# Performance work log

Hardware: AMD Instinct MI355X
Metric: run time of the kernel (lower is better)

The kernel has to match this reference:

```python
import jax, jax.numpy as jnp
import numpy as np

N_BONES = 8
NV = 14062
PARENTS = [-1, 0, 1, 2, 3, 4, 5, 6]  # kinematic chain


def rotvec_to_rotmat(rv):
    # rv: [..., 3] -> [..., 3, 3] via Rodrigues
    ang = jnp.sqrt(jnp.sum(rv * rv, axis=-1) + 1e-12)  # [...]
    k = rv / ang[..., None]
    kx, ky, kz = k[..., 0], k[..., 1], k[..., 2]
    z = jnp.zeros_like(kx)
    K = jnp.stack([
        jnp.stack([z, -kz, ky], -1),
        jnp.stack([kz, z, -kx], -1),
        jnp.stack([-ky, kx, z], -1)], -2)  # [...,3,3]
    s = jnp.sin(ang)[..., None, None]
    c = jnp.cos(ang)[..., None, None]
    I = jnp.eye(3, dtype=rv.dtype)
    return I + s * K + (1.0 - c) * (K @ K)


def bilinear_sample(img, gx, gy):
    # img: [H, W]; gx, gy: [B, Nv] normalized coords in [-1,1]
    # bilinear, border padding, align_corners=True (matches F.grid_sample)
    H, W = img.shape
    x = jnp.clip((gx + 1.0) * 0.5 * (W - 1), 0.0, W - 1.0)
    y = jnp.clip((gy + 1.0) * 0.5 * (H - 1), 0.0, H - 1.0)
    x0 = jnp.floor(x); y0 = jnp.floor(y)
    x0i = x0.astype(jnp.int32); y0i = y0.astype(jnp.int32)
    x1i = jnp.minimum(x0i + 1, W - 1); y1i = jnp.minimum(y0i + 1, H - 1)
    wx = x - x0; wy = y - y0
    v00 = img[y0i, x0i]; v01 = img[y0i, x1i]
    v10 = img[y1i, x0i]; v11 = img[y1i, x1i]
    return (v00 * (1 - wx) + v01 * wx) * (1 - wy) + (v10 * (1 - wx) + v11 * wx) * wy


def setup_inputs() -> dict:
    key = jax.random.key(0)
    ks = jax.random.split(key, 12)
    B = 256
    theta = jax.random.normal(ks[0], (B, N_BONES, 3), jnp.float32) * 0.3
    tau = jax.random.normal(ks[1], (B, 1), jnp.float32) * 0.1
    alpha = jax.random.uniform(ks[2], (B, 1), jnp.float32)
    bsw = jax.random.uniform(ks[3], (B, 55), jnp.float32)
    W = jax.random.uniform(ks[4], (N_BONES, NV), jnp.float32) + 1e-3
    W = W / W.sum(axis=0, keepdims=True)  # done in HACK.__init__
    T = jax.random.normal(ks[5], (NV, 3), jnp.float32)
    P = jax.random.normal(ks[6], (N_BONES, 3, 3, NV, 3), jnp.float32) * 0.01
    L = jax.random.uniform(ks[7], (1, 1, 256, 256), jnp.float32)
    ts = jax.random.normal(ks[8], (NV, 3), jnp.float32)
    # L2P: per-bone rigid transforms (rotation + small translation)
    rv = jax.random.normal(ks[9], (N_BONES, 3), jnp.float32) * 0.2
    R = rotvec_to_rotmat(rv)
    t = jax.random.normal(ks[10], (N_BONES, 3), jnp.float32) * 0.1
    L2P = jnp.tile(jnp.eye(4, dtype=jnp.float32), (N_BONES, 1, 1))
    L2P = L2P.at[:, :3, :3].set(R).at[:, :3, 3].set(t)
    E = jax.random.normal(ks[11], (55, NV, 3), jnp.float32) * 0.05
    uvgrid = jax.random.uniform(jax.random.fold_in(key, 99), (NV, 2), jnp.float32)
    return {"theta": theta, "tau": tau, "alpha": alpha, "bsw": bsw, "W": W,
            "T": T, "P": P, "L": L, "ts": ts, "L2P": L2P, "E": E, "uvgrid": uvgrid}


def reference(theta, tau, alpha, bsw, W, T, P, L, ts, L2P, E, uvgrid):
    B = theta.shape[0]
    R = rotvec_to_rotmat(theta)  # [B, Nb, 3, 3]
    # theta_matrix_zero: bone 0 subtracts itself (-> 0), others subtract I
    sub = jnp.concatenate([R[:, :1],
                           jnp.broadcast_to(jnp.eye(3, dtype=R.dtype), (B, N_BONES - 1, 3, 3))], axis=1)
    theta_zero = R - sub  # [B, Nb, 3, 3]
    # pose-corrective blendshapes: sum over (bone, i, j)
    P_theta = jnp.einsum('bnij,nijvk->bvk', theta_zero, P)  # [B, Nv, 3]

    # forward kinematics along chain: L2W_pose[i] = L2W_pose[parent] @ (L2P[i] @ local[i])
    local = jnp.tile(jnp.eye(4, dtype=R.dtype), (B, N_BONES, 1, 1))
    local = local.at[:, :, :3, :3].set(R)  # [B, Nb, 4, 4]
    mats = []
    for i in range(N_BONES):
        Ai = jnp.einsum('ij,bjk->bik', L2P[i], local[:, i])
        if PARENTS[i] >= 0:
            Ai = jnp.matmul(mats[PARENTS[i]], Ai)
        mats.append(Ai)
    L2W_pose = jnp.stack(mats, axis=1)  # [B, Nb, 4, 4]

    # rest-pose world-to-local (inverse bind matrices)
    rest = []
    for i in range(N_BONES):
        rest.append(L2P[i] if PARENTS[i] < 0 else rest[PARENTS[i]] @ L2P[i])
    W2L = jnp.linalg.inv(jnp.stack(rest))  # [Nb, 4, 4]

    W2L2pWs = jnp.einsum('bnij,njk->bnik', L2W_pose, W2L)  # [B, Nb, 4, 4]
    # skinning-weight contraction over bones -> per-vertex 4x4 transform
    M = jnp.einsum('bnij,nv->bvij', W2L2pWs, W)  # [B, Nv, 4, 4]

    # larynx displacement via grid_sample
    uv = uvgrid * 2.0 - 1.0  # [Nv, 2]
    gx = jnp.broadcast_to(uv[None, :, 0], (B, uv.shape[0]))
    gy = uv[None, :, 1] + tau * 2.0  # shift y by tau*2 (F.pad(tau*2,[1,0]))
    dist = bilinear_sample(L[0, 0], gx, gy)  # [B, Nv]
    L_tau = dist[:, :, None] * ts[None]  # [B, Nv, 3]

    T_theta = (T[None] + P_theta
               + jnp.einsum('bn,nvk->bvk', bsw, E)
               + L_tau * alpha[:, :, None])  # [B, Nv, 3]

    # homogeneous per-vertex 4x4 matvec, keep xyz
    T_transformed = (jnp.einsum('bvij,bvj->bvi', M[:, :, :3, :3], T_theta)
                     + M[:, :, :3, 3])
    return T_transformed
```

## Files before the change

kernel.cpp:

```cpp
#include <hip/hip_runtime.h>
#include <cmath>

#define NB     8
#define NVERT  14062
#define NV3    42186
#define BATCH  256
#define KP     63
#define KE     55
#define KPAD   120
#define KT     8
#define NSTEP  15
#define VT     32
#define BT     16

__device__ inline void mat4mul(const float* A, const float* B, float* C) {
#pragma unroll
  for (int i = 0; i < 4; i++)
#pragma unroll
    for (int j = 0; j < 4; j++) {
      float s = 0.f;
#pragma unroll
      for (int k = 0; k < 4; k++) s = fmaf(A[i*4+k], B[k*4+j], s);
      C[i*4+j] = s;
    }
}

__global__ void setup_kernel(const float* __restrict__ theta,
                             const float* __restrict__ bsw,
                             const float* __restrict__ L2P,
                             float* __restrict__ coef_t,
                             float* __restrict__ mats)
{
  int b = blockIdx.x * blockDim.x + threadIdx.x;
  if (b >= BATCH) return;

  float R[NB][9];
#pragma unroll
  for (int n = 0; n < NB; n++) {
    float rx = theta[(b*NB+n)*3+0];
    float ry = theta[(b*NB+n)*3+1];
    float rz = theta[(b*NB+n)*3+2];
    float ang = sqrtf(rx*rx + ry*ry + rz*rz + 1e-12f);
    float kx = rx/ang, ky = ry/ang, kz = rz/ang;
    float s = sinf(ang), c = cosf(ang);
    float K[9] = {0.f,-kz,ky,  kz,0.f,-kx,  -ky,kx,0.f};
    float K2[9];
#pragma unroll
    for (int i = 0; i < 3; i++)
#pragma unroll
      for (int j = 0; j < 3; j++) {
        float v = 0.f;
#pragma unroll
        for (int k = 0; k < 3; k++) v = fmaf(K[i*3+k], K[k*3+j], v);
        K2[i*3+j] = v;
      }
#pragma unroll
    for (int e = 0; e < 9; e++) {
      int i = e/3, j = e%3;
      R[n][e] = (i==j ? 1.f : 0.f) + s*K[e] + (1.f-c)*K2[e];
    }
  }

#pragma unroll
  for (int n = 1; n < NB; n++)
#pragma unroll
    for (int e = 0; e < 9; e++) {
      int i = e/3, j = e%3;
      coef_t[((n-1)*9+e)*BATCH + b] = R[n][e] - (i==j ? 1.f : 0.f);
    }
  for (int s2 = 0; s2 < KE; s2++)
    coef_t[(KP+s2)*BATCH + b] = bsw[b*KE + s2];
  coef_t[118*BATCH + b] = 0.f;
  coef_t[119*BATCH + b] = 0.f;

  float prevPose[16], prevRest[16];
#pragma unroll 1
  for (int n = 0; n < NB; n++) {
    float loc[16] = {R[n][0],R[n][1],R[n][2],0.f,
                     R[n][3],R[n][4],R[n][5],0.f,
                     R[n][6],R[n][7],R[n][8],0.f,
                     0.f,0.f,0.f,1.f};
    float A[16], pose[16], rest[16];
    mat4mul(&L2P[n*16], loc, A);
    if (n == 0) {
#pragma unroll
      for (int q = 0; q < 16; q++) { pose[q] = A[q]; rest[q] = L2P[q]; }
    } else {
      mat4mul(prevPose, A, pose);
      mat4mul(prevRest, &L2P[n*16], rest);
    }
    float w2l[16];
#pragma unroll
    for (int i = 0; i < 3; i++) {
#pragma unroll
      for (int j = 0; j < 3; j++) w2l[i*4+j] = rest[j*4+i];
      w2l[i*4+3] = -(rest[0*4+i]*rest[0*4+3] + rest[1*4+i]*rest[1*4+3] + rest[2*4+i]*rest[2*4+3]);
    }
    w2l[12]=0.f; w2l[13]=0.f; w2l[14]=0.f; w2l[15]=1.f;
    float skin[16];
    mat4mul(pose, w2l, skin);
#pragma unroll
    for (int i = 0; i < 3; i++)
#pragma unroll
      for (int j = 0; j < 4; j++)
        mats[(size_t)b*96 + n*12 + i*4 + j] = skin[i*4+j];
#pragma unroll
    for (int q = 0; q < 16; q++) { prevPose[q] = pose[q]; prevRest[q] = rest[q]; }
  }
}

__global__ __launch_bounds__(256) void gemm_kernel(
    const float* __restrict__ P, const float* __restrict__ E,
    const float* __restrict__ coef_t, float* __restrict__ Tth)
{
  __shared__ float dlds[KT][VT*3];
  __shared__ float clds[KT][BATCH];

  int tid = threadIdx.x;
  int vt  = tid & 7;
  int bg  = tid >> 3;
  int vbase = blockIdx.x * VT;
  size_t vbase3 = (size_t)vbase * 3;
  bool full = (vbase + VT) <= NVERT;

  float acc[8][12];
#pragma unroll
  for (int j = 0; j < 8; j++)
#pragma unroll
    for (int x = 0; x < 12; x++) acc[j][x] = 0.f;

  for (int step = 0; step < NSTEP; step++) {
    int c0 = step * KT;
    __syncthreads();
    if (tid < 192) {
      int r = tid / 24, q = tid % 24;
      int c = c0 + r;
      const float* src = (c < KP) ? (P + (size_t)(9 + c) * NV3)
                                  : (E + (size_t)((c < 118 ? c : 117) - KP) * NV3);
      if (full) {
        float4 v = *reinterpret_cast<const float4*>(src + vbase3 + q*4);
        *reinterpret_cast<float4*>(&dlds[r][q*4]) = v;
      } else {
#pragma unroll
        for (int u = 0; u < 4; u++) {
          size_t idx = vbase3 + q*4 + u;
          if (idx >= NV3) idx = NV3 - 1;
          dlds[r][q*4+u] = src[idx];
        }
      }
    }
#pragma unroll
    for (int rep = 0; rep < 2; rep++) {
      int f = tid + rep * 256;
      int r = f >> 6, pos = f & 63;
      float4 v = *reinterpret_cast<const float4*>(coef_t + (size_t)(c0+r)*BATCH + pos*4);
      *reinterpret_cast<float4*>(&clds[r][pos*4]) = v;
    }
    __syncthreads();

#pragma unroll
    for (int k = 0; k < KT; k++) {
      float4 ca = *reinterpret_cast<const float4*>(&clds[k][bg*8]);
      float4 cb = *reinterpret_cast<const float4*>(&clds[k][bg*8+4]);
      float4 d0 = *reinterpret_cast<const float4*>(&dlds[k][vt*12+0]);
      float4 d1 = *reinterpret_cast<const float4*>(&dlds[k][vt*12+4]);
      float4 d2 = *reinterpret_cast<const float4*>(&dlds[k][vt*12+8]);
      float cf[8] = {ca.x,ca.y,ca.z,ca.w, cb.x,cb.y,cb.z,cb.w};
      float dv[12] = {d0.x,d0.y,d0.z,d0.w, d1.x,d1.y,d1.z,d1.w, d2.x,d2.y,d2.z,d2.w};
#pragma unroll
      for (int j = 0; j < 8; j++)
#pragma unroll
        for (int x = 0; x < 12; x++)
          acc[j][x] = fmaf(cf[j], dv[x], acc[j][x]);
    }
  }

#pragma unroll
  for (int j = 0; j < 8; j++) {
    int b = bg*8 + j;
    if (full) {
      float4* dst = reinterpret_cast<float4*>(Tth + (size_t)b*NV3 + vbase3 + vt*12);
      float4 o0 = {acc[j][0],acc[j][1],acc[j][2],acc[j][3]};
      float4 o1 = {acc[j][4],acc[j][5],acc[j][6],acc[j][7]};
      float4 o2 = {acc[j][8],acc[j][9],acc[j][10],acc[j][11]};
      dst[0] = o0; dst[1] = o1; dst[2] = o2;
    } else {
#pragma unroll
      for (int x = 0; x < 12; x++) {
        size_t idx = vbase3 + vt*12 + x;
        if (idx < NV3) Tth[(size_t)b*NV3 + idx] = acc[j][x];
      }
    }
  }
}

__global__ __launch_bounds__(256) void epilogue_kernel(
    const float* __restrict__ Tth, const float* __restrict__ mats,
    const float* __restrict__ Wm,
    const float* __restrict__ T,
    const float* __restrict__ ts,
    const float* __restrict__ uvgrid,
    const float* __restrict__ Limg,
    const float* __restrict__ tau, const float* __restrict__ alpha,
    float* __restrict__ out)
{
  __shared__ float mlds[BT][96];
  __shared__ float tau_s[BT], alpha_s[BT];
  int tid = threadIdx.x;
  int b0 = blockIdx.y * BT;

  for (int f = tid; f < BT*24; f += 256) {
    int bb = f / 24, q = f % 24;
    float4 v = *reinterpret_cast<const float4*>(mats + (size_t)(b0+bb)*96 + q*4);
    *reinterpret_cast<float4*>(&mlds[bb][q*4]) = v;
  }
  if (tid < BT) { tau_s[tid] = tau[b0+tid]; alpha_s[tid] = alpha[b0+tid]; }
  __syncthreads();

  int v = blockIdx.x * 256 + tid;
  if (v >= NVERT) return;

  float W8[NB];
#pragma unroll
  for (int n = 0; n < NB; n++) W8[n] = Wm[(size_t)n*NVERT + v];
  float T0 = T[v*3+0], T1 = T[v*3+1], T2 = T[v*3+2];
  float s0 = ts[v*3+0], s1 = ts[v*3+1], s2 = ts[v*3+2];
  float uv0 = uvgrid[v*2+0], uv1 = uvgrid[v*2+1];

  float gx = uv0*2.f - 1.f;
  float xc = fminf(fmaxf((gx+1.f)*0.5f*255.f, 0.f), 255.f);
  float x0 = floorf(xc);
  int x0i = (int)x0;
  int x1i = min(x0i+1, 255);
  float wx = xc - x0;
  float gy_base = uv1*2.f - 1.f;

#pragma unroll 1
  for (int bi = 0; bi < BT; bi++) {
    int b = b0 + bi;
    float gy = gy_base + 2.f*tau_s[bi];
    float yc = fminf(fmaxf((gy+1.f)*0.5f*255.f, 0.f), 255.f);
    float y0 = floorf(yc);
    int y0i = (int)y0;
    int y1i = min(y0i+1, 255);
    float wy = yc - y0;
    float v00 = Limg[y0i*256 + x0i], v01 = Limg[y0i*256 + x1i];
    float v10 = Limg[y1i*256 + x0i], v11 = Limg[y1i*256 + x1i];
    float dist = (v00*(1.f-wx) + v01*wx)*(1.f-wy) + (v10*(1.f-wx) + v11*wx)*wy;
    float da = dist * alpha_s[bi];

    size_t tbase = (size_t)b*NV3 + (size_t)v*3;
    float xv0 = Tth[tbase+0] + T0 + da*s0;
    float xv1 = Tth[tbase+1] + T1 + da*s1;
    float xv2 = Tth[tbase+2] + T2 + da*s2;

    float o[3];
#pragma unroll
    for (int i = 0; i < 3; i++) {
      float r0=0.f, r1=0.f, r2=0.f, r3=0.f;
#pragma unroll
      for (int n = 0; n < NB; n++) {
        float4 m = *reinterpret_cast<const float4*>(&mlds[bi][n*12 + i*4]);
        float w = W8[n];
        r0 = fmaf(w, m.x, r0); r1 = fmaf(w, m.y, r1);
        r2 = fmaf(w, m.z, r2); r3 = fmaf(w, m.w, r3);
      }
      o[i] = fmaf(r0, xv0, fmaf(r1, xv1, fmaf(r2, xv2, r3)));
    }
    out[tbase+0] = o[0];
    out[tbase+1] = o[1];
    out[tbase+2] = o[2];
  }
}

extern "C" void kernel_launch(void* const* d_in, const int* in_sizes, int n_in,
                              void* d_out, int out_size, void* d_ws, size_t ws_size,
                              hipStream_t stream)
{
  const float* theta  = (const float*)d_in[0];
  const float* tau    = (const float*)d_in[1];
  const float* alpha  = (const float*)d_in[2];
  const float* bsw    = (const float*)d_in[3];
  const float* Wm     = (const float*)d_in[4];
  const float* T      = (const float*)d_in[5];
  const float* P      = (const float*)d_in[6];
  const float* L      = (const float*)d_in[7];
  const float* ts     = (const float*)d_in[8];
  const float* L2P    = (const float*)d_in[9];
  const float* E      = (const float*)d_in[10];
  const float* uvgrid = (const float*)d_in[11];
  float* out = (float*)d_out;

  float* Tth    = (float*)d_ws;
  float* coef_t = Tth + (size_t)BATCH * NV3;
  float* mats   = coef_t + (size_t)KPAD * BATCH;

  setup_kernel<<<dim3(4), dim3(64), 0, stream>>>(theta, bsw, L2P, coef_t, mats);
  gemm_kernel<<<dim3((NVERT + VT - 1) / VT), dim3(256), 0, stream>>>(P, E, coef_t, Tth);
  epilogue_kernel<<<dim3((NVERT + 255) / 256, BATCH / BT), dim3(256), 0, stream>>>(
      Tth, mats, Wm, T, ts, uvgrid, L, tau, alpha, out);
}
```

Baseline: 221.8 us.

## Fuse GEMM with skinning epilogue and register-prefetch next K tile

Merges the blendshape GEMM and the skinning epilogue into one kernel. The accumulated T_theta values stay in registers and the bilinear sample, weighted transform and output write happen in place, so the large intermediate Tth buffer is never written to or read back from global memory. The K loop also prefetches the next tile into registers while computing on the current LDS tile. The costs are higher register pressure (launch bounds now ask for 2 blocks per SM), per-thread global reads of the transform matrices, and strided 8-byte output stores.

```diff
diff --git a/kernel.cpp b/kernel.cpp
--- a/kernel.cpp
+++ b/kernel.cpp
@@ -11,7 +11,6 @@
 #define KT     8
 #define NSTEP  15
 #define VT     32
-#define BT     16
 
 __device__ inline void mat4mul(const float* A, const float* B, float* C) {
 #pragma unroll
@@ -109,9 +108,13 @@
   }
 }
 
-__global__ __launch_bounds__(256) void gemm_kernel(
+__global__ __launch_bounds__(256, 2) void fused_kernel(
     const float* __restrict__ P, const float* __restrict__ E,
-    const float* __restrict__ coef_t, float* __restrict__ Tth)
+    const float* __restrict__ coef_t, const float* __restrict__ matsg,
+    const float* __restrict__ Wm, const float* __restrict__ T,
+    const float* __restrict__ ts, const float* __restrict__ uvgrid,
+    const float* __restrict__ Limg, const float* __restrict__ tau,
+    const float* __restrict__ alpha, float* __restrict__ out)
 {
   __shared__ float dlds[KT][VT*3];
   __shared__ float clds[KT][BATCH];
@@ -122,6 +125,7 @@
   int vbase = blockIdx.x * VT;
   size_t vbase3 = (size_t)vbase * 3;
   bool full = (vbase + VT) <= NVERT;
+  int dr = tid / 24, dq = tid - dr*24;
 
   float acc[8][12];
 #pragma unroll
@@ -129,35 +133,47 @@
 #pragma unroll
     for (int x = 0; x < 12; x++) acc[j][x] = 0.f;
 
-  for (int step = 0; step < NSTEP; step++) {
-    int c0 = step * KT;
-    __syncthreads();
+  auto loadD = [&](int step, float4& d) {
     if (tid < 192) {
-      int r = tid / 24, q = tid % 24;
-      int c = c0 + r;
-      const float* src = (c < KP) ? (P + (size_t)(9 + c) * NV3)
-                                  : (E + (size_t)((c < 118 ? c : 117) - KP) * NV3);
+      int c = step*KT + dr;
+      const float* src = (c < KP) ? (P + (size_t)(9 + c)*NV3)
+                                  : (E + (size_t)((c < KP+KE ? c : KP+KE-1) - KP)*NV3);
       if (full) {
-        float4 v = *reinterpret_cast<const float4*>(src + vbase3 + q*4);
-        *reinterpret_cast<float4*>(&dlds[r][q*4]) = v;
+        d = *reinterpret_cast<const float4*>(src + vbase3 + dq*4);
       } else {
-#pragma unroll
-        for (int u = 0; u < 4; u++) {
-          size_t idx = vbase3 + q*4 + u;
+        float t0[4];
+#pragma unroll
+        for (int u2 = 0; u2 < 4; u2++) {
+          size_t idx = vbase3 + (size_t)dq*4 + u2;
           if (idx >= NV3) idx = NV3 - 1;
-          dlds[r][q*4+u] = src[idx];
+          t0[u2] = src[idx];
         }
-      }
-    }
-#pragma unroll
-    for (int rep = 0; rep < 2; rep++) {
-      int f = tid + rep * 256;
-      int r = f >> 6, pos = f & 63;
-      float4 v = *reinterpret_cast<const float4*>(coef_t + (size_t)(c0+r)*BATCH + pos*4);
-      *reinterpret_cast<float4*>(&clds[r][pos*4]) = v;
-    }
-    __syncthreads();
-
+        d = make_float4(t0[0], t0[1], t0[2], t0[3]);
+      }
+    }
+  };
+  auto loadC = [&](int step, float4& c0r, float4& c1r) {
+    int c0 = step*KT;
+    c0r = *reinterpret_cast<const float4*>(coef_t + (size_t)(c0 + (tid>>6))*BATCH + (tid&63)*4);
+    c1r = *reinterpret_cast<const float4*>(coef_t + (size_t)(c0 + 4 + (tid>>6))*BATCH + (tid&63)*4);
+  };
+  auto writeLDS = [&](const float4& d, const float4& c0r, const float4& c1r) {
+    if (tid < 192) *reinterpret_cast<float4*>(&dlds[0][0] + tid*4) = d;
+    *reinterpret_cast<float4*>(&clds[0][0] + tid*4) = c0r;
+    *reinterpret_cast<float4*>(&clds[0][0] + (tid+256)*4) = c1r;
+  };
+
+  {
+    float4 dreg, c0r, c1r;
+    loadD(0, dreg); loadC(0, c0r, c1r);
+    writeLDS(dreg, c0r, c1r);
+  }
+  __syncthreads();
+
+  for (int step = 0; step < NSTEP; ++step) {
+    float4 dn, cn0, cn1;
+    bool more = (step + 1 < NSTEP);
+    if (more) { loadD(step+1, dn); loadC(step+1, cn0, cn1); }
 #pragma unroll
     for (int k = 0; k < KT; k++) {
       float4 ca = *reinterpret_cast<const float4*>(&clds[k][bg*8]);
@@ -173,103 +189,102 @@
         for (int x = 0; x < 12; x++)
           acc[j][x] = fmaf(cf[j], dv[x], acc[j][x]);
     }
-  }
-
+    if (more) {
+      __syncthreads();
+      writeLDS(dn, cn0, cn1);
+      __syncthreads();
+    }
+  }
+
+  int v0 = vbase + vt*4;
+  float ta8[8], al8[8];
 #pragma unroll
   for (int j = 0; j < 8; j++) {
     int b = bg*8 + j;
-    if (full) {
-      float4* dst = reinterpret_cast<float4*>(Tth + (size_t)b*NV3 + vbase3 + vt*12);
-      float4 o0 = {acc[j][0],acc[j][1],acc[j][2],acc[j][3]};
-      float4 o1 = {acc[j][4],acc[j][5],acc[j][6],acc[j][7]};
-      float4 o2 = {acc[j][8],acc[j][9],acc[j][10],acc[j][11]};
-      dst[0] = o0; dst[1] = o1; dst[2] = o2;
-    } else {
-#pragma unroll
-      for (int x = 0; x < 12; x++) {
-        size_t idx = vbase3 + vt*12 + x;
-        if (idx < NV3) Tth[(size_t)b*NV3 + idx] = acc[j][x];
-      }
-    }
-  }
-}
-
-__global__ __launch_bounds__(256) void epilogue_kernel(
-    const float* __restrict__ Tth, const float* __restrict__ mats,
-    const float* __restrict__ Wm,
-    const float* __restrict__ T,
-    const float* __restrict__ ts,
-    const float* __restrict__ uvgrid,
-    const float* __restrict__ Limg,
-    const float* __restrict__ tau, const float* __restrict__ alpha,
-    float* __restrict__ out)
-{
-  __shared__ float mlds[BT][96];
-  __shared__ float tau_s[BT], alpha_s[BT];
-  int tid = threadIdx.x;
-  int b0 = blockIdx.y * BT;
-
-  for (int f = tid; f < BT*24; f += 256) {
-    int bb = f / 24, q = f % 24;
-    float4 v = *reinterpret_cast<const float4*>(mats + (size_t)(b0+bb)*96 + q*4);
-    *reinterpret_cast<float4*>(&mlds[bb][q*4]) = v;
-  }
-  if (tid < BT) { tau_s[tid] = tau[b0+tid]; alpha_s[tid] = alpha[b0+tid]; }
-  __syncthreads();
-
-  int v = blockIdx.x * 256 + tid;
-  if (v >= NVERT) return;
-
-  float W8[NB];
-#pragma unroll
-  for (int n = 0; n < NB; n++) W8[n] = Wm[(size_t)n*NVERT + v];
-  float T0 = T[v*3+0], T1 = T[v*3+1], T2 = T[v*3+2];
-  float s0 = ts[v*3+0], s1 = ts[v*3+1], s2 = ts[v*3+2];
-  float uv0 = uvgrid[v*2+0], uv1 = uvgrid[v*2+1];
-
-  float gx = uv0*2.f - 1.f;
-  float xc = fminf(fmaxf((gx+1.f)*0.5f*255.f, 0.f), 255.f);
-  float x0 = floorf(xc);
-  int x0i = (int)x0;
-  int x1i = min(x0i+1, 255);
-  float wx = xc - x0;
-  float gy_base = uv1*2.f - 1.f;
-
-#pragma unroll 1
-  for (int bi = 0; bi < BT; bi++) {
-    int b = b0 + bi;
-    float gy = gy_base + 2.f*tau_s[bi];
-    float yc = fminf(fmaxf((gy+1.f)*0.5f*255.f, 0.f), 255.f);
-    float y0 = floorf(yc);
-    int y0i = (int)y0;
-    int y1i = min(y0i+1, 255);
-    float wy = yc - y0;
-    float v00 = Limg[y0i*256 + x0i], v01 = Limg[y0i*256 + x1i];
-    float v10 = Limg[y1i*256 + x0i], v11 = Limg[y1i*256 + x1i];
-    float dist = (v00*(1.f-wx) + v01*wx)*(1.f-wy) + (v10*(1.f-wx) + v11*wx)*wy;
-    float da = dist * alpha_s[bi];
-
-    size_t tbase = (size_t)b*NV3 + (size_t)v*3;
-    float xv0 = Tth[tbase+0] + T0 + da*s0;
-    float xv1 = Tth[tbase+1] + T1 + da*s1;
-    float xv2 = Tth[tbase+2] + T2 + da*s2;
-
-    float o[3];
-#pragma unroll
-    for (int i = 0; i < 3; i++) {
-      float r0=0.f, r1=0.f, r2=0.f, r3=0.f;
-#pragma unroll
-      for (int n = 0; n < NB; n++) {
-        float4 m = *reinterpret_cast<const float4*>(&mlds[bi][n*12 + i*4]);
-        float w = W8[n];
-        r0 = fmaf(w, m.x, r0); r1 = fmaf(w, m.y, r1);
-        r2 = fmaf(w, m.z, r2); r3 = fmaf(w, m.w, r3);
-      }
-      o[i] = fmaf(r0, xv0, fmaf(r1, xv1, fmaf(r2, xv2, r3)));
-    }
-    out[tbase+0] = o[0];
-    out[tbase+1] = o[1];
-    out[tbase+2] = o[2];
+    ta8[j] = tau[b] * 2.f;
+    al8[j] = alpha[b];
+  }
+
+#pragma unroll
+  for (int uh = 0; uh < 2; uh++) {
+    float W8[2][NB], Tv[2][3], sv[2][3], wx2[2], gyb2[2];
+    int x02[2], x12[2];
+    bool val[2];
+#pragma unroll
+    for (int uu = 0; uu < 2; uu++) {
+      int v = v0 + uh*2 + uu;
+      val[uu] = (v < NVERT);
+      if (val[uu]) {
+#pragma unroll
+        for (int n = 0; n < NB; n++) W8[uu][n] = Wm[(size_t)n*NVERT + v];
+#pragma unroll
+        for (int c = 0; c < 3; c++) { Tv[uu][c] = T[v*3+c]; sv[uu][c] = ts[v*3+c]; }
+        float u0 = uvgrid[v*2+0], u1 = uvgrid[v*2+1];
+        float gx = u0*2.f - 1.f;
+        float xc = fminf(fmaxf((gx+1.f)*0.5f*255.f, 0.f), 255.f);
+        float xf = floorf(xc);
+        x02[uu] = (int)xf; x12[uu] = min(x02[uu]+1, 255);
+        wx2[uu] = xc - xf;
+        gyb2[uu] = u1*2.f - 1.f;
+      } else {
+#pragma unroll
+        for (int n = 0; n < NB; n++) W8[uu][n] = 0.f;
+#pragma unroll
+        for (int c = 0; c < 3; c++) { Tv[uu][c] = 0.f; sv[uu][c] = 0.f; }
+        wx2[uu] = 0.f; gyb2[uu] = 0.f; x02[uu] = 0; x12[uu] = 0;
+      }
+    }
+
+#pragma unroll
+    for (int j = 0; j < 8; j++) {
+      int b = bg*8 + j;
+      float xv[2][3];
+#pragma unroll
+      for (int uu = 0; uu < 2; uu++) {
+        float gy = gyb2[uu] + ta8[j];
+        float yc = fminf(fmaxf((gy+1.f)*0.5f*255.f, 0.f), 255.f);
+        float yf = floorf(yc);
+        int y0i = (int)yf;
+        int y1i = min(y0i+1, 255);
+        float wy = yc - yf;
+        float wx = wx2[uu];
+        float v00 = Limg[y0i*256 + x02[uu]], v01 = Limg[y0i*256 + x12[uu]];
+        float v10 = Limg[y1i*256 + x02[uu]], v11 = Limg[y1i*256 + x12[uu]];
+        float dist = (v00*(1.f-wx) + v01*wx)*(1.f-wy) + (v10*(1.f-wx) + v11*wx)*wy;
+        float da = dist * al8[j];
+        int xo = uh*6 + uu*3;
+        xv[uu][0] = acc[j][xo+0] + Tv[uu][0] + da*sv[uu][0];
+        xv[uu][1] = acc[j][xo+1] + Tv[uu][1] + da*sv[uu][1];
+        xv[uu][2] = acc[j][xo+2] + Tv[uu][2] + da*sv[uu][2];
+      }
+      float o[2][3];
+#pragma unroll
+      for (int i = 0; i < 3; i++) {
+        float c00=0.f,c01=0.f,c02=0.f,c03=0.f;
+        float c10=0.f,c11=0.f,c12=0.f,c13=0.f;
+#pragma unroll
+        for (int n = 0; n < NB; n++) {
+          float4 m = *reinterpret_cast<const float4*>(matsg + (size_t)b*96 + n*12 + i*4);
+          float wa = W8[0][n], wb = W8[1][n];
+          c00 = fmaf(wa, m.x, c00); c01 = fmaf(wa, m.y, c01);
+          c02 = fmaf(wa, m.z, c02); c03 = fmaf(wa, m.w, c03);
+          c10 = fmaf(wb, m.x, c10); c11 = fmaf(wb, m.y, c11);
+          c12 = fmaf(wb, m.z, c12); c13 = fmaf(wb, m.w, c13);
+        }
+        o[0][i] = fmaf(c00, xv[0][0], fmaf(c01, xv[0][1], fmaf(c02, xv[0][2], c03)));
+        o[1][i] = fmaf(c10, xv[1][0], fmaf(c11, xv[1][1], fmaf(c12, xv[1][2], c13)));
+      }
+      size_t obase = (size_t)b*NV3 + (size_t)(v0 + uh*2)*3;
+      if (val[0] && val[1]) {
+        float2* dst = reinterpret_cast<float2*>(out + obase);
+        dst[0] = make_float2(o[0][0], o[0][1]);
+        dst[1] = make_float2(o[0][2], o[1][0]);
+        dst[2] = make_float2(o[1][1], o[1][2]);
+      } else {
+        if (val[0]) { out[obase+0]=o[0][0]; out[obase+1]=o[0][1]; out[obase+2]=o[0][2]; }
+        if (val[1]) { out[obase+3]=o[1][0]; out[obase+4]=o[1][1]; out[obase+5]=o[1][2]; }
+      }
+    }
   }
 }
 
@@ -291,12 +306,10 @@
   const float* uvgrid = (const float*)d_in[11];
   float* out = (float*)d_out;
 
-  float* Tth    = (float*)d_ws;
-  float* coef_t = Tth + (size_t)BATCH * NV3;
+  float* coef_t = (float*)d_ws;
   float* mats   = coef_t + (size_t)KPAD * BATCH;
 
   setup_kernel<<<dim3(4), dim3(64), 0, stream>>>(theta, bsw, L2P, coef_t, mats);
-  gemm_kernel<<<dim3((NVERT + VT - 1) / VT), dim3(256), 0, stream>>>(P, E, coef_t, Tth);
-  epilogue_kernel<<<dim3((NVERT + 255) / 256, BATCH / BT), dim3(256), 0, stream>>>(
-      Tth, mats, Wm, T, ts, uvgrid, L, tau, alpha, out);
+  fused_kernel<<<dim3((NVERT + VT - 1) / VT), dim3(256), 0, stream>>>(
+      P, E, coef_t, mats, Wm, T, ts, uvgrid, L, tau, alpha, out);
 }
```

After: 268.3 us. 1.21x slower.
